# Optimization experiments

Hardware: AMD Instinct MI355X
Metric: run time of the kernel (lower is better)

The kernel has to match this reference:

```python
import jax, jax.numpy as jnp
import numpy as np

NUM_NODES = 16384
NUM_EDGES = 524288
D_IN = 128
D_OUT = 128


def setup_inputs() -> dict:
    key = jax.random.key(0)
    k1, k2, k3 = jax.random.split(key, 3)
    x = jax.random.normal(k1, (NUM_NODES, D_IN), dtype=jnp.float32)
    edge_index = jax.random.randint(k2, (2, NUM_EDGES), 0, NUM_NODES, dtype=jnp.int64)
    # Xavier-uniform-like W; B is zeros in the original init but we use small
    # random values so its branch contributes to the output numerically.
    limit = float(np.sqrt(6.0 / (D_IN + D_OUT)))
    W = jax.random.uniform(k3, (D_OUT, D_IN), dtype=jnp.float32, minval=-limit, maxval=limit)
    B = jax.random.normal(jax.random.fold_in(key, 7), (D_OUT, D_IN), dtype=jnp.float32) * 0.02
    return {"x": x, "edge_index": edge_index, "W": W, "B": B}


def reference(x, edge_index, W, B):
    n = x.shape[0]
    src = edge_index[0]
    dst = edge_index[1]
    # Dense adjacency: A[i, j] = 1 iff edge j -> i (duplicates collapse via set)
    A = jnp.zeros((n, n), dtype=x.dtype).at[dst, src].set(1.0)
    deg = A.sum(axis=1)                      # in-degree per node
    d_inv = 1.0 / jnp.maximum(deg, 1.0)      # clamp(min=1)
    agg = d_inv[:, None] * (A @ x)           # D_inv @ A @ x (diag as row scale)
    out = agg @ W.T + x @ B.T                # F.linear(.., W) + F.linear(x, B)
    return out
```

## Files before the change

### kernel.cpp

```cpp
#include <hip/hip_runtime.h>

#define NN  16384
#define NE  524288
#define D   128
#define CAP 128
#define GEMMB 512
#define FILLB 256

#define OFF_CNT  0u
#define OFF_SLAB 65536u
#define OFF_Y    4259840u
#define OFF_Z    8454144u

typedef __bf16 bf16x4 __attribute__((ext_vector_type(4)));
typedef __bf16 bf16x8 __attribute__((ext_vector_type(8)));
typedef float  f32x4  __attribute__((ext_vector_type(4)));
typedef unsigned short u16;

__global__ __launch_bounds__(256) void zero_k(int4* __restrict__ p) {
  p[blockIdx.x * 256 + threadIdx.x] = int4{0, 0, 0, 0};
}

__global__ __launch_bounds__(256, 2) void k1(const float* __restrict__ x,
                                             const int* __restrict__ ei,
                                             const float* __restrict__ W,
                                             const float* __restrict__ Bm,
                                             __bf16* __restrict__ y,
                                             float* __restrict__ z,
                                             int* __restrict__ cnt,
                                             u16* __restrict__ slab) {
  __shared__ __bf16 sA[32][40];
  __shared__ __bf16 sB[256][40];
  __shared__ int s_any;
  int b = blockIdx.x, t = threadIdx.x;

  if (b < GEMMB) {
    int l = t & 63, wid = t >> 6;
    int g = l >> 4, ln = l & 15;
    int mh = wid & 1, nh = wid >> 1;
    int row0 = b * 32;
    f32x4 acc[8];
#pragma unroll
    for (int nb = 0; nb < 8; ++nb) acc[nb] = f32x4{0.f, 0.f, 0.f, 0.f};

    for (int kc = 0; kc < 4; ++kc) {
      int kb = kc * 32;
      __syncthreads();
      {
        int rr = t >> 3, q = t & 7;
        float4 v = *(const float4*)&x[(size_t)(row0 + rr) * D + kb + q * 4];
        bf16x4 w = {(__bf16)v.x, (__bf16)v.y, (__bf16)v.z, (__bf16)v.w};
        *(bf16x4*)&sA[rr][q * 4] = w;
      }
#pragma unroll
      for (int u = 0; u < 8; ++u) {
        int f = u * 256 + t;
        int rr = f >> 3, q = f & 7;
        const float* Bp = (rr < 128) ? &W[(size_t)rr * D] : &Bm[(size_t)(rr - 128) * D];
        float4 v = *(const float4*)&Bp[kb + q * 4];
        bf16x4 w = {(__bf16)v.x, (__bf16)v.y, (__bf16)v.z, (__bf16)v.w};
        *(bf16x4*)&sB[rr][q * 4] = w;
      }
      __syncthreads();
      bf16x8 afr = *(const bf16x8*)&sA[mh * 16 + ln][g * 8];
#pragma unroll
      for (int nb = 0; nb < 8; ++nb) {
        bf16x8 bfr = *(const bf16x8*)&sB[nh * 128 + nb * 16 + ln][g * 8];
        acc[nb] = __builtin_amdgcn_mfma_f32_16x16x32_bf16(afr, bfr, acc[nb], 0, 0, 0);
      }
    }
    if (nh == 0) {
#pragma unroll
      for (int nb = 0; nb < 8; ++nb)
#pragma unroll
        for (int i = 0; i < 4; ++i)
          y[(size_t)(row0 + mh * 16 + g * 4 + i) * D + nb * 16 + ln] = (__bf16)acc[nb][i];
    } else {
#pragma unroll
      for (int nb = 0; nb < 8; ++nb)
#pragma unroll
        for (int i = 0; i < 4; ++i)
          z[(size_t)(row0 + mh * 16 + g * 4 + i) * D + nb * 16 + ln] = acc[nb][i];
    }
  } else {
    if (t == 0) s_any = 0;
    __syncthreads();
    int base = (b - GEMMB) * 2048;
    int any = 0;
#pragma unroll
    for (int u = 0; u < 8; ++u) any |= ei[2 * (base + u * 256 + t) + 1];
    if (any) atomicOr(&s_any, 1);
    __syncthreads();
    int is32 = s_any;
    int s_[8], d_[8], slot_[8];
#pragma unroll
    for (int u = 0; u < 8; ++u) {
      int i = base + u * 256 + t;
      s_[u] = is32 ? ei[i] : ei[2 * i];
      d_[u] = is32 ? ei[NE + i] : ei[2 * (NE + i)];
    }
#pragma unroll
    for (int u = 0; u < 8; ++u)
      slot_[u] = atomicAdd(&cnt[d_[u]], 1);
#pragma unroll
    for (int u = 0; u < 8; ++u)
      if (slot_[u] < CAP) slab[((size_t)d_[u] << 7) + slot_[u]] = (u16)s_[u];
  }
}

#define RPB 8
__global__ __launch_bounds__(256) void gather_k(const int* __restrict__ cnt,
                                                const u16* __restrict__ slab,
                                                const u16* __restrict__ y,
                                                const float* __restrict__ z,
                                                float* __restrict__ out) {
  __shared__ u16 s_col[RPB][CAP];
  __shared__ unsigned s_bm[RPB][512];
  int t = threadIdx.x, lane = t & 31, r = t >> 5;
  int row = blockIdx.x * RPB + r;
  int k = cnt[row];
  if (k > CAP) k = CAP;
  const u16* srow = slab + ((size_t)row << 7);
  for (int j = lane; j < k; j += 32) s_col[r][j] = srow[j];
#pragma unroll
  for (int u = 0; u < 16; ++u) s_bm[r][u * 32 + lane] = 0u;

  int lu = 0;
  for (int j = lane; j < k; j += 32) {
    unsigned c = s_col[r][j];
    unsigned bit = 1u << (c & 31);
    unsigned old = atomicOr(&s_bm[r][c >> 5], bit);
    int kp = (old & bit) ? 0 : 1;
    s_col[r][j] = (u16)(c | (kp << 15));
    lu += kp;
  }
#pragma unroll
  for (int off = 16; off; off >>= 1) lu += __shfl_xor(lu, off);
  float dinv = 1.0f / (float)(lu > 0 ? lu : 1);

  float4 a[8];
#pragma unroll
  for (int u = 0; u < 8; ++u) a[u] = float4{0.f, 0.f, 0.f, 0.f};
  const u16* yl = y + lane * 4;
#define ACCB(aa, vv, ff)                                                  \
  { aa.x += ff * __uint_as_float((vv).x << 16);                           \
    aa.y += ff * __uint_as_float((vv).x & 0xffff0000u);                   \
    aa.z += ff * __uint_as_float((vv).y << 16);                           \
    aa.w += ff * __uint_as_float((vv).y & 0xffff0000u); }
  int j = 0;
  for (; j + 8 <= k; j += 8) {
    float f[8];
    uint2 v[8];
#pragma unroll
    for (int u = 0; u < 8; ++u) {
      int cc = s_col[r][j + u];
      f[u] = (cc >> 15) ? 1.0f : 0.0f;
      v[u] = *(const uint2*)(yl + (size_t)(cc & 0x3FFF) * D);
    }
#pragma unroll
    for (int u = 0; u < 8; ++u) ACCB(a[u], v[u], f[u])
  }
  for (; j < k; ++j) {
    int cc = s_col[r][j];
    float f0 = (cc >> 15) ? 1.0f : 0.0f;
    uint2 v0 = *(const uint2*)(yl + (size_t)(cc & 0x3FFF) * D);
    ACCB(a[0], v0, f0)
  }
#undef ACCB
#pragma unroll
  for (int u = 4; u < 8; ++u) {
    a[u - 4].x += a[u].x; a[u - 4].y += a[u].y;
    a[u - 4].z += a[u].z; a[u - 4].w += a[u].w;
  }
  float4 zv = *(const float4*)(z + (size_t)row * D + lane * 4);
  float4 o;
  o.x = (a[0].x + a[1].x + a[2].x + a[3].x) * dinv + zv.x;
  o.y = (a[0].y + a[1].y + a[2].y + a[3].y) * dinv + zv.y;
  o.z = (a[0].z + a[1].z + a[2].z + a[3].z) * dinv + zv.z;
  o.w = (a[0].w + a[1].w + a[2].w + a[3].w) * dinv + zv.w;
  *(float4*)(out + (size_t)row * D + lane * 4) = o;
}

extern "C" void kernel_launch(void* const* d_in, const int* in_sizes, int n_in,
                              void* d_out, int out_size, void* d_ws, size_t ws_size,
                              hipStream_t stream) {
  const float* x = (const float*)d_in[0];
  const int* ei = (const int*)d_in[1];
  const float* W = (const float*)d_in[2];
  const float* Bm = (const float*)d_in[3];
  float* out = (float*)d_out;
  char* ws = (char*)d_ws;
  int* cnt = (int*)(ws + OFF_CNT);
  u16* slab = (u16*)(ws + OFF_SLAB);
  __bf16* y = (__bf16*)(ws + OFF_Y);
  float* z = (float*)(ws + OFF_Z);

  zero_k<<<16, 256, 0, stream>>>((int4*)ws);
  k1<<<GEMMB + FILLB, 256, 0, stream>>>(x, ei, W, Bm, y, z, cnt, slab);
  gather_k<<<NN / RPB, 256, 0, stream>>>(cnt, slab, (const u16*)y, z, out);
}
```

Measured before the change: 61.81 us.

## Pre-convert inputs to bf16 and restructure GEMM tiles with full weight in LDS

A new prep kernel zeroes the counters and converts x, W and B to bf16 in workspace, replacing the old zero kernel. The GEMM blocks now load the whole 256x128 bf16 weight once into LDS and read A fragments straight from global memory. Each wave computes both the y and z outputs for 16 rows, so there are 64 rows per block and the per-k-chunk syncs are gone. This adds an extra pass over x (read fp32, write bf16) and roughly 68KB of LDS per block, which limits occupancy. The z load in the gather kernel is hoisted to the start.

```diff
diff --git a/kernel.cpp b/kernel.cpp
--- a/kernel.cpp
+++ b/kernel.cpp
@@ -4,88 +4,97 @@
 #define NE  524288
 #define D   128
 #define CAP 128
-#define GEMMB 512
-#define FILLB 256
 
 #define OFF_CNT  0u
 #define OFF_SLAB 65536u
 #define OFF_Y    4259840u
 #define OFF_Z    8454144u
+#define OFF_XB   16842752u
+#define OFF_WB   21037056u
 
 typedef __bf16 bf16x4 __attribute__((ext_vector_type(4)));
 typedef __bf16 bf16x8 __attribute__((ext_vector_type(8)));
 typedef float  f32x4  __attribute__((ext_vector_type(4)));
 typedef unsigned short u16;
 
-__global__ __launch_bounds__(256) void zero_k(int4* __restrict__ p) {
-  p[blockIdx.x * 256 + threadIdx.x] = int4{0, 0, 0, 0};
-}
-
-__global__ __launch_bounds__(256, 2) void k1(const float* __restrict__ x,
+__global__ __launch_bounds__(256) void prep_k(const float* __restrict__ x,
+                                              const float* __restrict__ W,
+                                              const float* __restrict__ Bm,
+                                              __bf16* __restrict__ xb,
+                                              __bf16* __restrict__ wbg,
+                                              int4* __restrict__ cnt4) {
+  int b = blockIdx.x, t = threadIdx.x;
+  if (b < 16) {
+    cnt4[b * 256 + t] = int4{0, 0, 0, 0};
+  } else if (b < 48) {
+    int i = (b - 16) * 256 + t;
+    float4 v = (i < 4096) ? ((const float4*)W)[i] : ((const float4*)Bm)[i - 4096];
+    bf16x4 w = {(__bf16)v.x, (__bf16)v.y, (__bf16)v.z, (__bf16)v.w};
+    ((bf16x4*)wbg)[i] = w;
+  } else {
+    int i = (b - 48) * 256 + t;
+    float4 v = ((const float4*)x)[i];
+    bf16x4 w = {(__bf16)v.x, (__bf16)v.y, (__bf16)v.z, (__bf16)v.w};
+    ((bf16x4*)xb)[i] = w;
+  }
+}
+
+__global__ __launch_bounds__(256, 2) void k1(const u16* __restrict__ xb,
+                                             const u16* __restrict__ wbg,
                                              const int* __restrict__ ei,
-                                             const float* __restrict__ W,
-                                             const float* __restrict__ Bm,
                                              __bf16* __restrict__ y,
                                              float* __restrict__ z,
                                              int* __restrict__ cnt,
                                              u16* __restrict__ slab) {
-  __shared__ __bf16 sA[32][40];
-  __shared__ __bf16 sB[256][40];
+  __shared__ __align__(16) __bf16 swb[256][136];
   __shared__ int s_any;
   int b = blockIdx.x, t = threadIdx.x;
 
-  if (b < GEMMB) {
+  if (b < 256) {
     int l = t & 63, wid = t >> 6;
     int g = l >> 4, ln = l & 15;
-    int mh = wid & 1, nh = wid >> 1;
-    int row0 = b * 32;
-    f32x4 acc[8];
-#pragma unroll
-    for (int nb = 0; nb < 8; ++nb) acc[nb] = f32x4{0.f, 0.f, 0.f, 0.f};
-
+    int row0 = b * 64;
+
+#pragma unroll
+    for (int u = 0; u < 16; ++u) {
+      int e = u * 256 + t;
+      int rr = e >> 4, q = e & 15;
+      uint4 v = ((const uint4*)wbg)[e];
+      *(uint4*)&swb[rr][q * 8] = v;
+    }
+    __syncthreads();
+
+    f32x4 accY[8], accZ[8];
+#pragma unroll
+    for (int nb = 0; nb < 8; ++nb) {
+      accY[nb] = f32x4{0.f, 0.f, 0.f, 0.f};
+      accZ[nb] = f32x4{0.f, 0.f, 0.f, 0.f};
+    }
+    const u16* xrow = xb + (size_t)(row0 + wid * 16 + ln) * D;
+
+#pragma unroll
     for (int kc = 0; kc < 4; ++kc) {
-      int kb = kc * 32;
-      __syncthreads();
-      {
-        int rr = t >> 3, q = t & 7;
-        float4 v = *(const float4*)&x[(size_t)(row0 + rr) * D + kb + q * 4];
-        bf16x4 w = {(__bf16)v.x, (__bf16)v.y, (__bf16)v.z, (__bf16)v.w};
-        *(bf16x4*)&sA[rr][q * 4] = w;
+      bf16x8 afr = *(const bf16x8*)(xrow + kc * 32 + g * 8);
+#pragma unroll
+      for (int nb = 0; nb < 8; ++nb) {
+        bf16x8 bw = *(const bf16x8*)&swb[nb * 16 + ln][kc * 32 + g * 8];
+        accY[nb] = __builtin_amdgcn_mfma_f32_16x16x32_bf16(afr, bw, accY[nb], 0, 0, 0);
+        bf16x8 bb = *(const bf16x8*)&swb[128 + nb * 16 + ln][kc * 32 + g * 8];
+        accZ[nb] = __builtin_amdgcn_mfma_f32_16x16x32_bf16(afr, bb, accZ[nb], 0, 0, 0);
       }
-#pragma unroll
-      for (int u = 0; u < 8; ++u) {
-        int f = u * 256 + t;
-        int rr = f >> 3, q = f & 7;
-        const float* Bp = (rr < 128) ? &W[(size_t)rr * D] : &Bm[(size_t)(rr - 128) * D];
-        float4 v = *(const float4*)&Bp[kb + q * 4];
-        bf16x4 w = {(__bf16)v.x, (__bf16)v.y, (__bf16)v.z, (__bf16)v.w};
-        *(bf16x4*)&sB[rr][q * 4] = w;
+    }
+#pragma unroll
+    for (int nb = 0; nb < 8; ++nb)
+#pragma unroll
+      for (int i = 0; i < 4; ++i) {
+        size_t orow = (size_t)(row0 + wid * 16 + g * 4 + i) * D + nb * 16 + ln;
+        y[orow] = (__bf16)accY[nb][i];
+        z[orow] = accZ[nb][i];
       }
-      __syncthreads();
-      bf16x8 afr = *(const bf16x8*)&sA[mh * 16 + ln][g * 8];
-#pragma unroll
-      for (int nb = 0; nb < 8; ++nb) {
-        bf16x8 bfr = *(const bf16x8*)&sB[nh * 128 + nb * 16 + ln][g * 8];
-        acc[nb] = __builtin_amdgcn_mfma_f32_16x16x32_bf16(afr, bfr, acc[nb], 0, 0, 0);
-      }
-    }
-    if (nh == 0) {
-#pragma unroll
-      for (int nb = 0; nb < 8; ++nb)
-#pragma unroll
-        for (int i = 0; i < 4; ++i)
-          y[(size_t)(row0 + mh * 16 + g * 4 + i) * D + nb * 16 + ln] = (__bf16)acc[nb][i];
-    } else {
-#pragma unroll
-      for (int nb = 0; nb < 8; ++nb)
-#pragma unroll
-        for (int i = 0; i < 4; ++i)
-          z[(size_t)(row0 + mh * 16 + g * 4 + i) * D + nb * 16 + ln] = acc[nb][i];
-    }
   } else {
     if (t == 0) s_any = 0;
     __syncthreads();
-    int base = (b - GEMMB) * 2048;
+    int base = (b - 256) * 2048;
     int any = 0;
 #pragma unroll
     for (int u = 0; u < 8; ++u) any |= ei[2 * (base + u * 256 + t) + 1];
@@ -118,6 +127,7 @@
   __shared__ unsigned s_bm[RPB][512];
   int t = threadIdx.x, lane = t & 31, r = t >> 5;
   int row = blockIdx.x * RPB + r;
+  float4 zv = *(const float4*)(z + (size_t)row * D + lane * 4);
   int k = cnt[row];
   if (k > CAP) k = CAP;
   const u16* srow = slab + ((size_t)row << 7);
@@ -172,7 +182,6 @@
     a[u - 4].x += a[u].x; a[u - 4].y += a[u].y;
     a[u - 4].z += a[u].z; a[u - 4].w += a[u].w;
   }
-  float4 zv = *(const float4*)(z + (size_t)row * D + lane * 4);
   float4 o;
   o.x = (a[0].x + a[1].x + a[2].x + a[3].x) * dinv + zv.x;
   o.y = (a[0].y + a[1].y + a[2].y + a[3].y) * dinv + zv.y;
@@ -194,8 +203,10 @@
   u16* slab = (u16*)(ws + OFF_SLAB);
   __bf16* y = (__bf16*)(ws + OFF_Y);
   float* z = (float*)(ws + OFF_Z);
-
-  zero_k<<<16, 256, 0, stream>>>((int4*)ws);
-  k1<<<GEMMB + FILLB, 256, 0, stream>>>(x, ei, W, Bm, y, z, cnt, slab);
+  __bf16* xb = (__bf16*)(ws + OFF_XB);
+  __bf16* wbg = (__bf16*)(ws + OFF_WB);
+
+  prep_k<<<2096, 256, 0, stream>>>(x, W, Bm, xb, wbg, (int4*)cnt);
+  k1<<<512, 256, 0, stream>>>((const u16*)xb, (const u16*)wbg, ei, y, z, cnt, slab);
   gather_k<<<NN / RPB, 256, 0, stream>>>(cnt, slab, (const u16*)y, z, out);
 }
```

Result: faster. 58.34 us (-5.6%).
